# Performance work log

Hardware: AMD Instinct MI355X
Metric: run time of the kernel (lower is better)

Reference implementation:

```python
import jax, jax.numpy as jnp
import numpy as np

H = 1024  # hidden size

def lstm_cell(x, h, c, Wih, Whh, b):
    # torch gate order: i, f, g, o
    g = x @ Wih.T + h @ Whh.T + b
    i, f, gg, o = jnp.split(g, 4, axis=-1)
    c = jax.nn.sigmoid(f) * c + jax.nn.sigmoid(i) * jnp.tanh(gg)
    h = jax.nn.sigmoid(o) * jnp.tanh(c)
    return h, c

def lstm_layer(x, Wih, Whh, b):
    # x: [B, S, in] -> (y [B, S, H], h_last [B, H], c_last [B, H])
    B = x.shape[0]
    h0 = jnp.zeros((B, H), x.dtype)
    def step(carry, xt):
        h, c = carry
        h, c = lstm_cell(xt, h, c, Wih, Whh, b)
        return (h, c), h
    (h, c), ys = jax.lax.scan(step, (h0, h0), jnp.swapaxes(x, 0, 1))
    return jnp.swapaxes(ys, 0, 1), h, c

def setup_inputs() -> dict:
    key = jax.random.key(0)
    ks = iter(jax.random.split(key, 24))
    V, E, B, Ss, St = 32000, 512, 32, 64, 64
    s = 0.05
    d = {
        'source': jax.random.randint(next(ks), (B, Ss), 0, V),
        'prev_outputs': jax.random.randint(next(ks), (B, St), 0, V),
        'emb': jax.random.normal(next(ks), (V, E)) * s,
        'enc_Wih0': jax.random.normal(next(ks), (4*H, E)) * s,
        'enc_Whh0': jax.random.normal(next(ks), (4*H, H)) * s,
        'enc_b0': jax.random.normal(next(ks), (4*H,)) * s,
        'enc_Wih1': jax.random.normal(next(ks), (4*H, H)) * s,
        'enc_Whh1': jax.random.normal(next(ks), (4*H, H)) * s,
        'enc_b1': jax.random.normal(next(ks), (4*H,)) * s,
        'dec_Wih0': jax.random.normal(next(ks), (4*H, E + H)) * s,
        'dec_Whh0': jax.random.normal(next(ks), (4*H, H)) * s,
        'dec_b0': jax.random.normal(next(ks), (4*H,)) * s,
        'dec_Wih1': jax.random.normal(next(ks), (4*H, H)) * s,
        'dec_Whh1': jax.random.normal(next(ks), (4*H, H)) * s,
        'dec_b1': jax.random.normal(next(ks), (4*H,)) * s,
        'Wk': jax.random.normal(next(ks), (H, H)) * s,
        'bk': jax.random.normal(next(ks), (H,)) * s,
        'Wh': jax.random.normal(next(ks), (V, H)) * s,
        'bh': jax.random.normal(next(ks), (V,)) * s,
    }
    return d

def reference(source, prev_outputs, emb, enc_Wih0, enc_Whh0, enc_b0,
              enc_Wih1, enc_Whh1, enc_b1, dec_Wih0, dec_Whh0, dec_b0,
              dec_Wih1, dec_Whh1, dec_b1, Wk, bk, Wh, bh):
    src_e = emb[source]          # [B, Ss, E]
    tgt_e = emb[prev_outputs]    # [B, St, E]
    y0, h0e, c0e = lstm_layer(src_e, enc_Wih0, enc_Whh0, enc_b0)
    enc_out, h1e, c1e = lstm_layer(y0, enc_Wih1, enc_Whh1, enc_b1)
    h = jnp.stack([h0e, h1e])    # [L, B, H]
    c = jnp.stack([c0e, c1e])
    attn_key = enc_out @ Wk.T + bk  # constant across decoder steps

    def step(carry, xt):  # xt: [B, E]
        h, c = carry
        q = h[-1]                                        # [B, H]
        scores = jnp.einsum('bh,bsh->bs', q, attn_key)   # [B, Ss]
        probs = jax.nn.softmax(scores, axis=-1)
        ctx = jnp.einsum('bs,bsh->bh', probs, enc_out)   # [B, H]
        inp = jnp.concatenate([xt, ctx], axis=-1)        # [B, E+H]
        h0n, c0n = lstm_cell(inp, h[0], c[0], dec_Wih0, dec_Whh0, dec_b0)
        h1n, c1n = lstm_cell(h0n, h[1], c[1], dec_Wih1, dec_Whh1, dec_b1)
        logits_t = h1n @ Wh.T + bh                       # [B, V]
        return (jnp.stack([h0n, h1n]), jnp.stack([c0n, c1n])), logits_t

    _, logits = jax.lax.scan(step, (h, c), jnp.swapaxes(tgt_e, 0, 1))
    return jnp.swapaxes(logits, 0, 1)  # [B, St, V]
```

## Files before the change

### kernel.cpp

```cpp
#include <hip/hip_runtime.h>
#include <cmath>

typedef short bs8 __attribute__((ext_vector_type(8)));
typedef float f32x4 __attribute__((ext_vector_type(4)));
typedef __attribute__((address_space(3))) unsigned lds_uint;
typedef __attribute__((address_space(1))) const unsigned gbl_uint;

#define NV 32000
#define SLOTH (32 * 1024)

__device__ __forceinline__ float b2f(unsigned short u) {
  union { unsigned int i; float f; } v; v.i = ((unsigned int)u) << 16; return v.f;
}
__device__ __forceinline__ unsigned short f2b(float f) {
  unsigned int u = __float_as_uint(f);
  return (unsigned short)((u + 0x7FFFu + ((u >> 16) & 1u)) >> 16);
}
__device__ __forceinline__ f32x4 mfma16(bs8 a, bs8 b, f32x4 c) {
  return __builtin_amdgcn_mfma_f32_16x16x32_bf16(a, b, c, 0, 0, 0);
}

__device__ __forceinline__ void waitN(const unsigned* slots, int n, unsigned target) {
  if (threadIdx.x < 64) {
    for (;;) {
      unsigned mn = 0xffffffffu;
      for (int i = threadIdx.x; i < n; i += 64) {
        unsigned v = __hip_atomic_load(slots + (size_t)i * 4,
                                       __ATOMIC_RELAXED, __HIP_MEMORY_SCOPE_AGENT);
        mn = mn < v ? mn : v;
      }
#pragma unroll
      for (int off = 32; off; off >>= 1) {
        unsigned o = __shfl_xor(mn, off);
        mn = mn < o ? mn : o;
      }
      if (mn >= target) break;
      __builtin_amdgcn_s_sleep(2);
    }
  }
  __syncthreads();
}
__device__ __forceinline__ void signal_slot(unsigned* slot, unsigned val) {
  __syncthreads();
  if (threadIdx.x == 0)
    __hip_atomic_store(slot, val, __ATOMIC_RELAXED, __HIP_MEMORY_SCOPE_AGENT);
}

__device__ __forceinline__ void mfma_half8(
    const unsigned short* __restrict__ A, const unsigned short* __restrict__ W,
    int u0, f32x4& acc0, f32x4& acc1) {
  int tid = threadIdx.x;
  int w = tid >> 6, l = tid & 63;
  int col = l & 15;
  int kb = w * 128 + (l >> 4) * 8;
  size_t wrow = (size_t)(col >> 2) * 1024 + u0 + (col & 3);
  const unsigned short* ap = A + (size_t)col * 1024 + kb;
  const unsigned short* wp = W + wrow * 1024 + kb;
#pragma unroll
  for (int kk = 0; kk < 128; kk += 32) {
    bs8 b1 = *(const bs8*)(wp + kk);
    acc0 = mfma16(*(const bs8*)(ap + kk), b1, acc0);
    acc1 = mfma16(*(const bs8*)(ap + 16 * 1024 + kk), b1, acc1);
  }
}
__device__ __forceinline__ void red_write8(f32x4 acc0, f32x4 acc1, float (*red)[32][17]) {
  int tid = threadIdx.x;
  int w = tid >> 6, l = tid & 63, col = l & 15;
#pragma unroll
  for (int r = 0; r < 4; r++) {
    red[w][(l >> 4) * 4 + r][col] = acc0[r];
    red[w][16 + (l >> 4) * 4 + r][col] = acc1[r];
  }
  __syncthreads();
}
template <int NW, int AH>
__device__ __forceinline__ void cell_finish(
    int u0, float (*red)[32][17],
    const float* __restrict__ gxrow, const float* __restrict__ bias,
    const float* __restrict__ cprev,
    unsigned short* __restrict__ hout, float* __restrict__ cout) {
  int tid = threadIdx.x;
  if (tid < 128) {
    int b_ = tid >> 2, ul = tid & 3, u = u0 + ul;
    float s0 = 0.f, s1 = 0.f, s2 = 0.f, s3 = 0.f;
#pragma unroll
    for (int ww = 0; ww < NW; ww++) {
      s0 += red[ww][b_][ul];      s1 += red[ww][b_][4 + ul];
      s2 += red[ww][b_][8 + ul];  s3 += red[ww][b_][12 + ul];
    }
    if (gxrow) {
      const float* gp = gxrow + (size_t)b_ * 4096 + u;
      s0 += gp[0]; s1 += gp[1024]; s2 += gp[2048]; s3 += gp[3072];
    }
    if (bias) {
      s0 += bias[u]; s1 += bias[u + 1024]; s2 += bias[u + 2048]; s3 += bias[u + 3072];
    }
    float si = 1.f / (1.f + expf(-s0));
    float sf = 1.f / (1.f + expf(-s1));
    float tg = tanhf(s2);
    float so = 1.f / (1.f + expf(-s3));
    float cn = sf * cprev[b_ * 1024 + u] + si * tg;
    float hn = so * tanhf(cn);
    cout[b_ * 1024 + u] = cn;
    unsigned hv = (unsigned)f2b(hn);
    unsigned ho = __shfl_down(hv, 1);
    if (AH) {
      if (!(ul & 1)) {
        unsigned packed = hv | (ho << 16);
        __hip_atomic_store((unsigned*)hout + ((size_t)b_ * 512 + (u0 >> 1) + (ul >> 1)),
                           packed, __ATOMIC_RELAXED, __HIP_MEMORY_SCOPE_AGENT);
      }
    } else {
      hout[b_ * 1024 + u] = (unsigned short)hv;
    }
  }
}

__global__ __launch_bounds__(512) void enc_diag(
    int d,
    const unsigned short* __restrict__ wH0, const float* __restrict__ gx0,
    unsigned short* __restrict__ y0h, float* __restrict__ c0h,
    const unsigned short* __restrict__ wE1, const unsigned short* __restrict__ wH1,
    const float* __restrict__ eb1,
    unsigned short* __restrict__ y1h, float* __restrict__ c1h) {
  __shared__ float red[8][32][17];
  if (blockIdx.x < 256) {
    if (d >= 64) return;
    int u0 = blockIdx.x * 4;
    f32x4 a0 = {0.f, 0.f, 0.f, 0.f}, a1 = {0.f, 0.f, 0.f, 0.f};
    mfma_half8(y0h + (size_t)d * SLOTH, wH0, u0, a0, a1);
    red_write8(a0, a1, red);
    cell_finish<8, 0>(u0, red, gx0 + (size_t)d * 131072, nullptr,
                      c0h + (size_t)d * SLOTH,
                      y0h + (size_t)(d + 1) * SLOTH, c0h + (size_t)(d + 1) * SLOTH);
  } else {
    if (d < 1) return;
    int j = d - 1, u0 = (blockIdx.x - 256) * 4;
    f32x4 a0 = {0.f, 0.f, 0.f, 0.f}, a1 = {0.f, 0.f, 0.f, 0.f};
    mfma_half8(y0h + (size_t)(j + 1) * SLOTH, wE1, u0, a0, a1);
    mfma_half8(y1h + (size_t)j * SLOTH, wH1, u0, a0, a1);
    red_write8(a0, a1, red);
    cell_finish<8, 0>(u0, red, nullptr, eb1, c1h + (size_t)j * SLOTH,
                      y1h + (size_t)(j + 1) * SLOTH, c1h + (size_t)(j + 1) * SLOTH);
  }
}

__device__ __forceinline__ void mfma_half_lds(
    const unsigned short* __restrict__ A, const unsigned short* wl,
    f32x4& acc0, f32x4& acc1) {
  int tid = threadIdx.x;
  int w = tid >> 6, l = tid & 63;
  int col = l & 15;
  int kb = w * 256 + (l >> 4) * 8;
  const unsigned short* ap = A + (size_t)col * 1024 + kb;
  const unsigned short* wp = wl + col * 1032 + kb;
#pragma unroll
  for (int kk = 0; kk < 256; kk += 32) {
    bs8 b1 = *(const bs8*)(wp + kk);
    acc0 = mfma16(*(const bs8*)(ap + kk), b1, acc0);
    acc1 = mfma16(*(const bs8*)(ap + 16 * 1024 + kk), b1, acc1);
  }
}
__device__ __forceinline__ void red_write4(f32x4 acc0, f32x4 acc1, float (*red)[32][17]) {
  int tid = threadIdx.x;
  int w = tid >> 6, l = tid & 63, col = l & 15;
#pragma unroll
  for (int r = 0; r < 4; r++) {
    red[w][(l >> 4) * 4 + r][col] = acc0[r];
    red[w][16 + (l >> 4) * 4 + r][col] = acc1[r];
  }
  __syncthreads();
}

__global__ __launch_bounds__(256, 2) void dec_persist(
    const unsigned short* __restrict__ ak, const unsigned short* __restrict__ enc,
    const float* __restrict__ gxd,
    const unsigned short* __restrict__ wDh0, const unsigned short* __restrict__ wD0c,
    const unsigned short* __restrict__ wD1, const unsigned short* __restrict__ wDh1,
    const float* __restrict__ db1, unsigned short* __restrict__ ctxb,
    unsigned short* __restrict__ dh0, float* __restrict__ dc0,
    unsigned short* __restrict__ dh1, float* __restrict__ dc1,
    unsigned* __restrict__ flags) {
  __shared__ unsigned short wl[2][16 * 1032];
  __shared__ float red[4][32][17];
  __shared__ float qs[1024];
  __shared__ float sc[64];
  int bid = blockIdx.x, tid = threadIdx.x;
  int cell0 = (bid < 256);
  int u0 = (bid & 255) * 4;
  unsigned* fH0 = flags;
  unsigned* fH1 = flags + 1024;
  unsigned* fP  = flags + 2048;
  {
    const unsigned short* W0 = cell0 ? wDh0 : wD1;
    const unsigned short* W1 = cell0 ? wD0c : wDh1;
    for (int i = tid; i < 2048; i += 256) {
      int c = i >> 7, c8 = (i & 127) * 8;
      size_t grow = (size_t)(c >> 2) * 1024 + u0 + (c & 3);
      *(bs8*)&wl[0][c * 1032 + c8] = *(const bs8*)(W0 + grow * 1024 + c8);
      *(bs8*)&wl[1][c * 1032 + c8] = *(const bs8*)(W1 + grow * 1024 + c8);
    }
    __syncthreads();
  }
  if (cell0) {
    for (int t = 0; t < 64; t++) {
      if (t > 0) waitN(fH0, 256, (unsigned)t);
      f32x4 a0 = {0.f, 0.f, 0.f, 0.f}, a1 = {0.f, 0.f, 0.f, 0.f};
      mfma_half_lds(dh0 + (size_t)t * SLOTH, wl[0], a0, a1);
      waitN(fP, 32, (unsigned)(t + 1));
      mfma_half_lds(ctxb + (size_t)t * SLOTH, wl[1], a0, a1);
      red_write4(a0, a1, red);
      cell_finish<4, 1>(u0, red, gxd + (size_t)t * 131072, nullptr,
                        dc0 + (size_t)t * SLOTH,
                        dh0 + (size_t)(t + 1) * SLOTH, dc0 + (size_t)(t + 1) * SLOTH);
      signal_slot(fH0 + (size_t)bid * 4, (unsigned)(t + 1));
    }
  } else {
    int ab = bid - 256;
    for (int t = 0; t < 64; t++) {
      if (t > 0) waitN(fH1, 256, (unsigned)t);
      if (ab < 32) {
        {
          ushort4 u4 = *(const ushort4*)(dh1 + (size_t)t * SLOTH + (size_t)ab * 1024 + tid * 4);
          qs[tid * 4 + 0] = b2f(u4.x); qs[tid * 4 + 1] = b2f(u4.y);
          qs[tid * 4 + 2] = b2f(u4.z); qs[tid * 4 + 3] = b2f(u4.w);
        }
        __syncthreads();
        int w = tid >> 6, l = tid & 63;
        for (int ss = 0; ss < 16; ss++) {
          int s = w * 16 + ss;
          const unsigned short* kr = ak + (size_t)(s * 32 + ab) * 1024;
          float p = 0.f;
#pragma unroll
          for (int i = 0; i < 4; i++) {
            int e = (l + i * 64) * 4;
            ushort4 u4 = *(const ushort4*)&kr[e];
            p += qs[e] * b2f(u4.x) + qs[e + 1] * b2f(u4.y)
               + qs[e + 2] * b2f(u4.z) + qs[e + 3] * b2f(u4.w);
          }
          for (int off = 32; off; off >>= 1) p += __shfl_down(p, off);
          if (l == 0) sc[s] = p;
        }
        __syncthreads();
        if (tid < 64) {
          float v = sc[tid], m = v;
          for (int off = 32; off; off >>= 1) m = fmaxf(m, __shfl_xor(m, off));
          float e = expf(v - m), su = e;
          for (int off = 32; off; off >>= 1) su += __shfl_xor(su, off);
          sc[tid] = e / su;
        }
        __syncthreads();
        {
          int h4 = tid * 4;
          float a0 = 0.f, a1 = 0.f, a2 = 0.f, a3 = 0.f;
#pragma unroll 8
          for (int s = 0; s < 64; s++) {
            float p = sc[s];
            ushort4 u4 = *(const ushort4*)&enc[(size_t)(s * 32 + ab) * 1024 + h4];
            a0 += p * b2f(u4.x); a1 += p * b2f(u4.y);
            a2 += p * b2f(u4.z); a3 += p * b2f(u4.w);
          }
          unsigned* cp = (unsigned*)(ctxb + (size_t)t * SLOTH) + ab * 512 + tid * 2;
          __hip_atomic_store(cp, (unsigned)f2b(a0) | ((unsigned)f2b(a1) << 16),
                             __ATOMIC_RELAXED, __HIP_MEMORY_SCOPE_AGENT);
          __hip_atomic_store(cp + 1, (unsigned)f2b(a2) | ((unsigned)f2b(a3) << 16),
                             __ATOMIC_RELAXED, __HIP_MEMORY_SCOPE_AGENT);
        }
        signal_slot(fP + (size_t)ab * 4, (unsigned)(t + 1));
      }
      f32x4 a0 = {0.f, 0.f, 0.f, 0.f}, a1 = {0.f, 0.f, 0.f, 0.f};
      mfma_half_lds(dh1 + (size_t)t * SLOTH, wl[1], a0, a1);
      waitN(fH0, 256, (unsigned)(t + 1));
      mfma_half_lds(dh0 + (size_t)(t + 1) * SLOTH, wl[0], a0, a1);
      red_write4(a0, a1, red);
      cell_finish<4, 1>(u0, red, nullptr, db1, dc1 + (size_t)t * SLOTH,
                        dh1 + (size_t)(t + 1) * SLOTH, dc1 + (size_t)(t + 1) * SLOTH);
      signal_slot(fH1 + (size_t)(bid - 256) * 4, (unsigned)(t + 1));
    }
  }
}

struct CvtDesc { const float* src; unsigned short* dst; int total8, cols, ld, col0, blk0; };
struct CvtArgs { CvtDesc d[11]; };
__global__ __launch_bounds__(256) void cvt_all(CvtArgs a) {
  int blk = blockIdx.x, seg = 0;
#pragma unroll
  for (int i = 1; i < 11; i++) if (blk >= a.d[i].blk0) seg = i;
  CvtDesc d = a.d[seg];
  int idx = (blk - d.blk0) * 256 + threadIdx.x;
  if (idx >= d.total8) return;
  int cpr = d.cols >> 3;
  int r = idx / cpr, c8 = (idx - r * cpr) * 8;
  const float* s = d.src + (size_t)r * d.ld + d.col0 + c8;
  float4 x = *(const float4*)s, y = *(const float4*)(s + 4);
  unsigned short o[8] = {f2b(x.x), f2b(x.y), f2b(x.z), f2b(x.w),
                         f2b(y.x), f2b(y.y), f2b(y.z), f2b(y.w)};
  *(bs8*)(d.dst + (size_t)r * d.cols + c8) = *(bs8*)o;
}

__global__ __launch_bounds__(256) void embed_kernel(
    const int* __restrict__ src, const int* __restrict__ prev,
    const float* __restrict__ emb,
    unsigned short* __restrict__ se, unsigned short* __restrict__ te) {
  int idx = blockIdx.x * 256 + threadIdx.x;
  int half = idx >> 17;
  int r = (idx >> 6) & 2047, c8 = (idx & 63) * 8;
  int s = r >> 5, b = r & 31;
  const int* tok = half ? prev : src;
  unsigned short* dst = half ? te : se;
  int t = tok[b * 64 + s];
  const float* e = emb + (size_t)t * 512 + c8;
  float4 a = *(const float4*)e, bb = *(const float4*)(e + 4);
  unsigned short o[8] = {f2b(a.x), f2b(a.y), f2b(a.z), f2b(a.w),
                         f2b(bb.x), f2b(bb.y), f2b(bb.z), f2b(bb.w)};
  *(bs8*)(dst + (size_t)r * 512 + c8) = *(bs8*)o;
}

#define NFLAGS 4096
__global__ __launch_bounds__(256) void zero_init(
    unsigned short* y0h, unsigned short* y1h, float* c0h, float* c1h,
    unsigned* flags) {
  int i = blockIdx.x * 256 + threadIdx.x;
  y0h[i] = 0; y1h[i] = 0; c0h[i] = 0.f; c1h[i] = 0.f;
  if (i < NFLAGS) flags[i] = 0u;
}
__global__ __launch_bounds__(256) void init_dec(
    const unsigned short* __restrict__ y0f, const unsigned short* __restrict__ y1f,
    const float* __restrict__ c0f, const float* __restrict__ c1f,
    unsigned short* dh0, unsigned short* dh1, float* dc0, float* dc1) {
  int i = blockIdx.x * 256 + threadIdx.x;
  dh0[i] = y0f[i]; dh1[i] = y1f[i]; dc0[i] = c0f[i]; dc1[i] = c1f[i];
}

template <int OUTMODE>
__global__ __launch_bounds__(256) void gemm_bf16(
    const unsigned short* __restrict__ A, int lda,
    const unsigned short* __restrict__ B, int ldb,
    const float* __restrict__ bias, void* __restrict__ Cp, int ldc, int K) {
  __shared__ unsigned short As[128 * 64];
  __shared__ unsigned short Bs[128 * 64];
  int tid = threadIdx.x;
  int m0, n0;
  if (OUTMODE == 1) {
    int nwg = gridDim.x * gridDim.y;
    int orig = blockIdx.y * gridDim.x + blockIdx.x;
    int q = nwg >> 3;
    int wg = (orig & 7) * q + (orig >> 3);
    m0 = (wg % gridDim.x) * 128;
    n0 = (wg / gridDim.x) * 128;
  } else {
    m0 = blockIdx.x * 128; n0 = blockIdx.y * 128;
  }
  int w = tid >> 6, l = tid & 63;
  int wr = w >> 1, wc = w & 1;
  int swz = ((l & 7) * 8) ^ ((l >> 3) * 8);
  f32x4 acc[4][4];
#pragma unroll
  for (int i = 0; i < 4; i++)
#pragma unroll
    for (int j = 0; j < 4; j++)
#pragma unroll
      for (int r = 0; r < 4; r++) acc[i][j][r] = 0.f;

  for (int k0 = 0; k0 < K; k0 += 64) {
    __syncthreads();
#pragma unroll
    for (int i = 0; i < 4; i++) {
      int rb = w * 8 + i * 32;
      const unsigned short* ga = A + (size_t)(m0 + rb + (l >> 3)) * lda + k0 + swz;
      __builtin_amdgcn_global_load_lds((gbl_uint*)ga, (lds_uint*)&As[rb * 64], 16, 0, 0);
      const unsigned short* gb = B + (size_t)(n0 + rb + (l >> 3)) * ldb + k0 + swz;
      __builtin_amdgcn_global_load_lds((gbl_uint*)gb, (lds_uint*)&Bs[rb * 64], 16, 0, 0);
    }
    __syncthreads();
#pragma unroll
    for (int kk = 0; kk < 2; kk++) {
      bs8 af[4], bfr[4];
#pragma unroll
      for (int i = 0; i < 4; i++) {
        int R = wr * 64 + i * 16 + (l & 15);
        af[i] = *(const bs8*)&As[R * 64 + ((kk * 32 + (l >> 4) * 8) ^ ((R & 7) * 8))];
      }
#pragma unroll
      for (int j = 0; j < 4; j++) {
        int R = wc * 64 + j * 16 + (l & 15);
        bfr[j] = *(const bs8*)&Bs[R * 64 + ((kk * 32 + (l >> 4) * 8) ^ ((R & 7) * 8))];
      }
#pragma unroll
      for (int i = 0; i < 4; i++)
#pragma unroll
        for (int j = 0; j < 4; j++)
          acc[i][j] = mfma16(af[i], bfr[j], acc[i][j]);
    }
  }
#pragma unroll
  for (int i = 0; i < 4; i++) {
    int mrow = m0 + wr * 64 + i * 16 + (l >> 4) * 4;
#pragma unroll
    for (int j = 0; j < 4; j++) {
      int n = n0 + wc * 64 + j * 16 + (l & 15);
      float bb = bias ? bias[n] : 0.f;
#pragma unroll
      for (int r = 0; r < 4; r++) {
        int m = mrow + r;
        float v = acc[i][j][r] + bb;
        if (OUTMODE == 1)
          ((float*)Cp)[(size_t)(m & 31) * (64ull * NV) + (size_t)(m >> 5) * NV + n] = v;
        else if (OUTMODE == 2)
          ((unsigned short*)Cp)[(size_t)m * ldc + n] = f2b(v);
        else
          ((float*)Cp)[(size_t)m * ldc + n] = v;
      }
    }
  }
}

extern "C" void kernel_launch(void* const* d_in, const int* in_sizes, int n_in,
                              void* d_out, int out_size, void* d_ws, size_t ws_size,
                              hipStream_t stream) {
  (void)in_sizes; (void)n_in; (void)out_size; (void)ws_size;
  const int*   src   = (const int*)d_in[0];
  const int*   prev  = (const int*)d_in[1];
  const float* emb   = (const float*)d_in[2];
  const float* eWih0 = (const float*)d_in[3];
  const float* eWhh0 = (const float*)d_in[4];
  const float* eb0   = (const float*)d_in[5];
  const float* eWih1 = (const float*)d_in[6];
  const float* eWhh1 = (const float*)d_in[7];
  const float* eb1   = (const float*)d_in[8];
  const float* dWih0 = (const float*)d_in[9];
  const float* dWhh0 = (const float*)d_in[10];
  const float* db0   = (const float*)d_in[11];
  const float* dWih1 = (const float*)d_in[12];
  const float* dWhh1 = (const float*)d_in[13];
  const float* db1   = (const float*)d_in[14];
  const float* Wk    = (const float*)d_in[15];
  const float* bk    = (const float*)d_in[16];
  const float* Wh    = (const float*)d_in[17];
  const float* bh    = (const float*)d_in[18];
  float* out = (float*)d_out;

  char* p = (char*)d_ws;
  auto alloc = [&](size_t bytes) {
    char* r = p; p += (bytes + 255) & ~(size_t)255; return r;
  };
  float* gx0 = (float*)alloc(2048ull * 4096 * 4);
  float* gxd = (float*)alloc(2048ull * 4096 * 4);
  float* c0h = (float*)alloc(65ull * SLOTH * 4);
  float* c1h = (float*)alloc(65ull * SLOTH * 4);
  float* dc0 = (float*)alloc(65ull * SLOTH * 4);
  float* dc1 = (float*)alloc(65ull * SLOTH * 4);
  unsigned short* y0h  = (unsigned short*)alloc(65ull * SLOTH * 2);
  unsigned short* y1h  = (unsigned short*)alloc(65ull * SLOTH * 2);
  unsigned short* dh0  = (unsigned short*)alloc(65ull * SLOTH * 2);
  unsigned short* dh1  = (unsigned short*)alloc(65ull * SLOTH * 2);
  unsigned short* ctxb = (unsigned short*)alloc(64ull * SLOTH * 2);
  unsigned short* se   = (unsigned short*)alloc(2048ull * 512 * 2);
  unsigned short* te   = (unsigned short*)alloc(2048ull * 512 * 2);
  unsigned short* ak   = (unsigned short*)alloc(2048ull * 1024 * 2);
  unsigned short* wE0  = (unsigned short*)alloc(4096ull * 512 * 2);
  unsigned short* wH0  = (unsigned short*)alloc(4096ull * 1024 * 2);
  unsigned short* wE1  = (unsigned short*)alloc(4096ull * 1024 * 2);
  unsigned short* wH1  = (unsigned short*)alloc(4096ull * 1024 * 2);
  unsigned short* wD0x = (unsigned short*)alloc(4096ull * 512 * 2);
  unsigned short* wD0c = (unsigned short*)alloc(4096ull * 1024 * 2);
  unsigned short* wDh0 = (unsigned short*)alloc(4096ull * 1024 * 2);
  unsigned short* wD1  = (unsigned short*)alloc(4096ull * 1024 * 2);
  unsigned short* wDh1 = (unsigned short*)alloc(4096ull * 1024 * 2);
  unsigned short* wK   = (unsigned short*)alloc(1024ull * 1024 * 2);
  unsigned short* wV   = (unsigned short*)alloc((size_t)NV * 1024 * 2);
  unsigned* flags = (unsigned*)alloc((size_t)NFLAGS * 4);

  CvtArgs ca; int nb = 0, ci = 0;
  auto addcvt = [&](const float* s, unsigned short* d, int rows, int cols, int ld, int c0) {
    int t8 = rows * cols / 8;
    ca.d[ci++] = CvtDesc{s, d, t8, cols, ld, c0, nb};
    nb += (t8 + 255) / 256;
  };
  addcvt(eWih0, wE0, 4096, 512, 512, 0);
  addcvt(eWhh0, wH0, 4096, 1024, 1024, 0);
  addcvt(eWih1, wE1, 4096, 1024, 1024, 0);
  addcvt(eWhh1, wH1, 4096, 1024, 1024, 0);
  addcvt(dWih0, wD0x, 4096, 512, 1536, 0);
  addcvt(dWih0, wD0c, 4096, 1024, 1536, 512);
  addcvt(dWhh0, wDh0, 4096, 1024, 1024, 0);
  addcvt(dWih1, wD1, 4096, 1024, 1024, 0);
  addcvt(dWhh1, wDh1, 4096, 1024, 1024, 0);
  addcvt(Wk, wK, 1024, 1024, 1024, 0);
  addcvt(Wh, wV, NV, 1024, 1024, 0);
  cvt_all<<<nb, 256, 0, stream>>>(ca);

  zero_init<<<128, 256, 0, stream>>>(y0h, y1h, c0h, c1h, flags);
  embed_kernel<<<1024, 256, 0, stream>>>(src, prev, emb, se, te);

  gemm_bf16<0><<<dim3(16, 32), 256, 0, stream>>>(se, 512, wE0, 512, eb0, gx0, 4096, 512);
  gemm_bf16<0><<<dim3(16, 32), 256, 0, stream>>>(te, 512, wD0x, 512, db0, gxd, 4096, 512);

  for (int d = 0; d <= 64; d++)
    enc_diag<<<512, 512, 0, stream>>>(d, wH0, gx0, y0h, c0h, wE1, wH1, eb1, y1h, c1h);

  gemm_bf16<2><<<dim3(16, 8), 256, 0, stream>>>(y1h + SLOTH, 1024, wK, 1024, bk, ak, 1024, 1024);
  init_dec<<<128, 256, 0, stream>>>(y0h + 64 * SLOTH, y1h + 64 * SLOTH,
                                    c0h + 64 * SLOTH, c1h + 64 * SLOTH,
                                    dh0, dh1, dc0, dc1);
  dec_persist<<<512, 256, 0, stream>>>(ak, y1h + SLOTH, gxd, wDh0, wD0c, wD1, wDh1,
                                       db1, ctxb, dh0, dc0, dh1, dc1, flags);
  gemm_bf16<1><<<dim3(16, 250), 256, 0, stream>>>(dh1 + SLOTH, 1024, wV, 1024, bh, out, NV, 1024);
}
```

Before: 2.800 ms.

## Split decoder batch into two 16-row cohorts with separate flags to pipeline steps

The persistent decoder kernel now processes the 32-row batch as two independent cohorts of 16 rows. Each cohort has its own ready flags for layer-0 hidden, layer-1 hidden and the attention context. Each cohort's matmul, gate activation and signal can proceed as soon as its own inputs are ready, so the attention and the next layer can start on cohort A while cohort B is still in flight. The cost is twice as many flag waits and signals, plus block barriers per step, and each MFMA pass reuses the loaded weights across fewer rows.

```diff
diff --git a/kernel.cpp b/kernel.cpp
--- a/kernel.cpp
+++ b/kernel.cpp
@@ -145,31 +145,63 @@
   }
 }
 
-__device__ __forceinline__ void mfma_half_lds(
+__device__ __forceinline__ void mfma_cohort(
     const unsigned short* __restrict__ A, const unsigned short* wl,
-    f32x4& acc0, f32x4& acc1) {
+    int X, f32x4& acc) {
   int tid = threadIdx.x;
   int w = tid >> 6, l = tid & 63;
   int col = l & 15;
   int kb = w * 256 + (l >> 4) * 8;
-  const unsigned short* ap = A + (size_t)col * 1024 + kb;
+  const unsigned short* ap = A + (size_t)(X * 16 + col) * 1024 + kb;
   const unsigned short* wp = wl + col * 1032 + kb;
 #pragma unroll
-  for (int kk = 0; kk < 256; kk += 32) {
-    bs8 b1 = *(const bs8*)(wp + kk);
-    acc0 = mfma16(*(const bs8*)(ap + kk), b1, acc0);
-    acc1 = mfma16(*(const bs8*)(ap + 16 * 1024 + kk), b1, acc1);
-  }
-}
-__device__ __forceinline__ void red_write4(f32x4 acc0, f32x4 acc1, float (*red)[32][17]) {
+  for (int kk = 0; kk < 256; kk += 32)
+    acc = mfma16(*(const bs8*)(ap + kk), *(const bs8*)(wp + kk), acc);
+}
+__device__ __forceinline__ void red_write1(f32x4 acc, float (*red)[16][17]) {
   int tid = threadIdx.x;
   int w = tid >> 6, l = tid & 63, col = l & 15;
 #pragma unroll
-  for (int r = 0; r < 4; r++) {
-    red[w][(l >> 4) * 4 + r][col] = acc0[r];
-    red[w][16 + (l >> 4) * 4 + r][col] = acc1[r];
-  }
+  for (int r = 0; r < 4; r++) red[w][(l >> 4) * 4 + r][col] = acc[r];
   __syncthreads();
+}
+__device__ __forceinline__ void finish16(
+    int u0, int X, float (*red)[16][17],
+    const float* __restrict__ gxrow, const float* __restrict__ bias,
+    const float* __restrict__ cprev,
+    unsigned short* __restrict__ hout, float* __restrict__ cout) {
+  int tid = threadIdx.x;
+  if (tid < 64) {
+    int b_ = tid >> 2, ul = tid & 3, u = u0 + ul;
+    int bm = X * 16 + b_;
+    float s0 = 0.f, s1 = 0.f, s2 = 0.f, s3 = 0.f;
+#pragma unroll
+    for (int ww = 0; ww < 4; ww++) {
+      s0 += red[ww][b_][ul];      s1 += red[ww][b_][4 + ul];
+      s2 += red[ww][b_][8 + ul];  s3 += red[ww][b_][12 + ul];
+    }
+    if (gxrow) {
+      const float* gp = gxrow + (size_t)bm * 4096 + u;
+      s0 += gp[0]; s1 += gp[1024]; s2 += gp[2048]; s3 += gp[3072];
+    }
+    if (bias) {
+      s0 += bias[u]; s1 += bias[u + 1024]; s2 += bias[u + 2048]; s3 += bias[u + 3072];
+    }
+    float si = 1.f / (1.f + expf(-s0));
+    float sf = 1.f / (1.f + expf(-s1));
+    float tg = tanhf(s2);
+    float so = 1.f / (1.f + expf(-s3));
+    float cn = sf * cprev[bm * 1024 + u] + si * tg;
+    float hn = so * tanhf(cn);
+    cout[bm * 1024 + u] = cn;
+    unsigned hv = (unsigned)f2b(hn);
+    unsigned ho = __shfl_down(hv, 1);
+    if (!(ul & 1)) {
+      unsigned packed = hv | (ho << 16);
+      __hip_atomic_store((unsigned*)hout + ((size_t)bm * 512 + (u0 >> 1) + (ul >> 1)),
+                         packed, __ATOMIC_RELAXED, __HIP_MEMORY_SCOPE_AGENT);
+    }
+  }
 }
 
 __global__ __launch_bounds__(256, 2) void dec_persist(
@@ -182,15 +214,18 @@
     unsigned short* __restrict__ dh1, float* __restrict__ dc1,
     unsigned* __restrict__ flags) {
   __shared__ unsigned short wl[2][16 * 1032];
-  __shared__ float red[4][32][17];
+  __shared__ float red[4][16][17];
   __shared__ float qs[1024];
   __shared__ float sc[64];
   int bid = blockIdx.x, tid = threadIdx.x;
   int cell0 = (bid < 256);
   int u0 = (bid & 255) * 4;
-  unsigned* fH0 = flags;
-  unsigned* fH1 = flags + 1024;
-  unsigned* fP  = flags + 2048;
+  unsigned* fH0A = flags;
+  unsigned* fH0B = flags + 1024;
+  unsigned* fH1A = flags + 2048;
+  unsigned* fH1B = flags + 3072;
+  unsigned* fPA  = flags + 4096;
+  unsigned* fPB  = flags + 4160;
   {
     const unsigned short* W0 = cell0 ? wDh0 : wD1;
     const unsigned short* W1 = cell0 ? wD0c : wDh1;
@@ -204,22 +239,32 @@
   }
   if (cell0) {
     for (int t = 0; t < 64; t++) {
-      if (t > 0) waitN(fH0, 256, (unsigned)t);
-      f32x4 a0 = {0.f, 0.f, 0.f, 0.f}, a1 = {0.f, 0.f, 0.f, 0.f};
-      mfma_half_lds(dh0 + (size_t)t * SLOTH, wl[0], a0, a1);
-      waitN(fP, 32, (unsigned)(t + 1));
-      mfma_half_lds(ctxb + (size_t)t * SLOTH, wl[1], a0, a1);
-      red_write4(a0, a1, red);
-      cell_finish<4, 1>(u0, red, gxd + (size_t)t * 131072, nullptr,
-                        dc0 + (size_t)t * SLOTH,
-                        dh0 + (size_t)(t + 1) * SLOTH, dc0 + (size_t)(t + 1) * SLOTH);
-      signal_slot(fH0 + (size_t)bid * 4, (unsigned)(t + 1));
+      f32x4 accA = {0.f, 0.f, 0.f, 0.f}, accB = {0.f, 0.f, 0.f, 0.f};
+      if (t > 0) waitN(fH0A, 256, (unsigned)t);
+      mfma_cohort(dh0 + (size_t)t * SLOTH, wl[0], 0, accA);
+      if (t > 0) waitN(fH0B, 256, (unsigned)t);
+      mfma_cohort(dh0 + (size_t)t * SLOTH, wl[0], 1, accB);
+      waitN(fPA, 16, (unsigned)(t + 1));
+      mfma_cohort(ctxb + (size_t)t * SLOTH, wl[1], 0, accA);
+      red_write1(accA, red);
+      finish16(u0, 0, red, gxd + (size_t)t * 131072, nullptr,
+               dc0 + (size_t)t * SLOTH,
+               dh0 + (size_t)(t + 1) * SLOTH, dc0 + (size_t)(t + 1) * SLOTH);
+      signal_slot(fH0A + (size_t)bid * 4, (unsigned)(t + 1));
+      waitN(fPB, 16, (unsigned)(t + 1));
+      mfma_cohort(ctxb + (size_t)t * SLOTH, wl[1], 1, accB);
+      red_write1(accB, red);
+      finish16(u0, 1, red, gxd + (size_t)t * 131072, nullptr,
+               dc0 + (size_t)t * SLOTH,
+               dh0 + (size_t)(t + 1) * SLOTH, dc0 + (size_t)(t + 1) * SLOTH);
+      signal_slot(fH0B + (size_t)bid * 4, (unsigned)(t + 1));
     }
   } else {
     int ab = bid - 256;
     for (int t = 0; t < 64; t++) {
-      if (t > 0) waitN(fH1, 256, (unsigned)t);
       if (ab < 32) {
+        unsigned* fH1X = (ab < 16) ? fH1A : fH1B;
+        waitN(fH1X, 256, (unsigned)t);
         {
           ushort4 u4 = *(const ushort4*)(dh1 + (size_t)t * SLOTH + (size_t)ab * 1024 + tid * 4);
           qs[tid * 4 + 0] = b2f(u4.x); qs[tid * 4 + 1] = b2f(u4.y);
@@ -266,16 +311,26 @@
           __hip_atomic_store(cp + 1, (unsigned)f2b(a2) | ((unsigned)f2b(a3) << 16),
                              __ATOMIC_RELAXED, __HIP_MEMORY_SCOPE_AGENT);
         }
-        signal_slot(fP + (size_t)ab * 4, (unsigned)(t + 1));
-      }
-      f32x4 a0 = {0.f, 0.f, 0.f, 0.f}, a1 = {0.f, 0.f, 0.f, 0.f};
-      mfma_half_lds(dh1 + (size_t)t * SLOTH, wl[1], a0, a1);
-      waitN(fH0, 256, (unsigned)(t + 1));
-      mfma_half_lds(dh0 + (size_t)(t + 1) * SLOTH, wl[0], a0, a1);
-      red_write4(a0, a1, red);
-      cell_finish<4, 1>(u0, red, nullptr, db1, dc1 + (size_t)t * SLOTH,
-                        dh1 + (size_t)(t + 1) * SLOTH, dc1 + (size_t)(t + 1) * SLOTH);
-      signal_slot(fH1 + (size_t)(bid - 256) * 4, (unsigned)(t + 1));
+        unsigned* fPX = (ab < 16) ? fPA : fPB;
+        signal_slot(fPX + (size_t)(ab & 15) * 4, (unsigned)(t + 1));
+      }
+      f32x4 accA = {0.f, 0.f, 0.f, 0.f}, accB = {0.f, 0.f, 0.f, 0.f};
+      if (t > 0) waitN(fH1A, 256, (unsigned)t);
+      mfma_cohort(dh1 + (size_t)t * SLOTH, wl[1], 0, accA);
+      if (t > 0) waitN(fH1B, 256, (unsigned)t);
+      mfma_cohort(dh1 + (size_t)t * SLOTH, wl[1], 1, accB);
+      waitN(fH0A, 256, (unsigned)(t + 1));
+      mfma_cohort(dh0 + (size_t)(t + 1) * SLOTH, wl[0], 0, accA);
+      red_write1(accA, red);
+      finish16(u0, 0, red, nullptr, db1, dc1 + (size_t)t * SLOTH,
+               dh1 + (size_t)(t + 1) * SLOTH, dc1 + (size_t)(t + 1) * SLOTH);
+      signal_slot(fH1A + (size_t)(bid - 256) * 4, (unsigned)(t + 1));
+      waitN(fH0B, 256, (unsigned)(t + 1));
+      mfma_cohort(dh0 + (size_t)(t + 1) * SLOTH, wl[0], 1, accB);
+      red_write1(accB, red);
+      finish16(u0, 1, red, nullptr, db1, dc1 + (size_t)t * SLOTH,
+               dh1 + (size_t)(t + 1) * SLOTH, dc1 + (size_t)(t + 1) * SLOTH);
+      signal_slot(fH1B + (size_t)(bid - 256) * 4, (unsigned)(t + 1));
     }
   }
 }
@@ -316,7 +371,7 @@
   *(bs8*)(dst + (size_t)r * 512 + c8) = *(bs8*)o;
 }
 
-#define NFLAGS 4096
+#define NFLAGS 4224
 __global__ __launch_bounds__(256) void zero_init(
     unsigned short* y0h, unsigned short* y1h, float* c0h, float* c1h,
     unsigned* flags) {
```

After: 2.838 ms. Within noise of the previous version (+1.4%).

## Replace per-step encoder kernel launches with a persistent flag-synchronized kernel

Applied to the files above, without the earlier changes.

The encoder wavefront, which used 65 separate kernel launches each holding a diagonal step, becomes one persistent kernel. Each block caches its slice of the recurrent weights in LDS once and then synchronizes step-to-step through global flag counters, using the same scheme the decoder already uses. This removes launch overhead and the per-step weight reloads from global memory. In exchange it relies on all 512 blocks being co-resident (two per CU) and adds spin-wait polling, which risks deadlock if occupancy falls short.

```diff
diff --git a/kernel.cpp b/kernel.cpp
--- a/kernel.cpp
+++ b/kernel.cpp
@@ -46,24 +46,23 @@
     __hip_atomic_store(slot, val, __ATOMIC_RELAXED, __HIP_MEMORY_SCOPE_AGENT);
 }
 
-__device__ __forceinline__ void mfma_half8(
-    const unsigned short* __restrict__ A, const unsigned short* __restrict__ W,
-    int u0, f32x4& acc0, f32x4& acc1) {
+__device__ __forceinline__ void mfma_half_lds(
+    const unsigned short* __restrict__ A, const unsigned short* wl,
+    f32x4& acc0, f32x4& acc1) {
   int tid = threadIdx.x;
   int w = tid >> 6, l = tid & 63;
   int col = l & 15;
-  int kb = w * 128 + (l >> 4) * 8;
-  size_t wrow = (size_t)(col >> 2) * 1024 + u0 + (col & 3);
+  int kb = w * 256 + (l >> 4) * 8;
   const unsigned short* ap = A + (size_t)col * 1024 + kb;
-  const unsigned short* wp = W + wrow * 1024 + kb;
-#pragma unroll
-  for (int kk = 0; kk < 128; kk += 32) {
+  const unsigned short* wp = wl + col * 1032 + kb;
+#pragma unroll
+  for (int kk = 0; kk < 256; kk += 32) {
     bs8 b1 = *(const bs8*)(wp + kk);
     acc0 = mfma16(*(const bs8*)(ap + kk), b1, acc0);
     acc1 = mfma16(*(const bs8*)(ap + 16 * 1024 + kk), b1, acc1);
   }
 }
-__device__ __forceinline__ void red_write8(f32x4 acc0, f32x4 acc1, float (*red)[32][17]) {
+__device__ __forceinline__ void red_write4(f32x4 acc0, f32x4 acc1, float (*red)[32][17]) {
   int tid = threadIdx.x;
   int w = tid >> 6, l = tid & 63, col = l & 15;
 #pragma unroll
@@ -73,8 +72,7 @@
   }
   __syncthreads();
 }
-template <int NW, int AH>
-__device__ __forceinline__ void cell_finish(
+__device__ __forceinline__ void cell_finish4(
     int u0, float (*red)[32][17],
     const float* __restrict__ gxrow, const float* __restrict__ bias,
     const float* __restrict__ cprev,
@@ -84,7 +82,7 @@
     int b_ = tid >> 2, ul = tid & 3, u = u0 + ul;
     float s0 = 0.f, s1 = 0.f, s2 = 0.f, s3 = 0.f;
 #pragma unroll
-    for (int ww = 0; ww < NW; ww++) {
+    for (int ww = 0; ww < 4; ww++) {
       s0 += red[ww][b_][ul];      s1 += red[ww][b_][4 + ul];
       s2 += red[ww][b_][8 + ul];  s3 += red[ww][b_][12 + ul];
     }
@@ -104,72 +102,61 @@
     cout[b_ * 1024 + u] = cn;
     unsigned hv = (unsigned)f2b(hn);
     unsigned ho = __shfl_down(hv, 1);
-    if (AH) {
-      if (!(ul & 1)) {
-        unsigned packed = hv | (ho << 16);
-        __hip_atomic_store((unsigned*)hout + ((size_t)b_ * 512 + (u0 >> 1) + (ul >> 1)),
-                           packed, __ATOMIC_RELAXED, __HIP_MEMORY_SCOPE_AGENT);
-      }
-    } else {
-      hout[b_ * 1024 + u] = (unsigned short)hv;
-    }
-  }
-}
-
-__global__ __launch_bounds__(512) void enc_diag(
-    int d,
+    if (!(ul & 1)) {
+      unsigned packed = hv | (ho << 16);
+      __hip_atomic_store((unsigned*)hout + ((size_t)b_ * 512 + (u0 >> 1) + (ul >> 1)),
+                         packed, __ATOMIC_RELAXED, __HIP_MEMORY_SCOPE_AGENT);
+    }
+  }
+}
+
+__global__ __launch_bounds__(256, 2) void enc_persist(
     const unsigned short* __restrict__ wH0, const float* __restrict__ gx0,
     unsigned short* __restrict__ y0h, float* __restrict__ c0h,
     const unsigned short* __restrict__ wE1, const unsigned short* __restrict__ wH1,
     const float* __restrict__ eb1,
-    unsigned short* __restrict__ y1h, float* __restrict__ c1h) {
-  __shared__ float red[8][32][17];
-  if (blockIdx.x < 256) {
-    if (d >= 64) return;
-    int u0 = blockIdx.x * 4;
-    f32x4 a0 = {0.f, 0.f, 0.f, 0.f}, a1 = {0.f, 0.f, 0.f, 0.f};
-    mfma_half8(y0h + (size_t)d * SLOTH, wH0, u0, a0, a1);
-    red_write8(a0, a1, red);
-    cell_finish<8, 0>(u0, red, gx0 + (size_t)d * 131072, nullptr,
-                      c0h + (size_t)d * SLOTH,
-                      y0h + (size_t)(d + 1) * SLOTH, c0h + (size_t)(d + 1) * SLOTH);
+    unsigned short* __restrict__ y1h, float* __restrict__ c1h,
+    unsigned* __restrict__ fE, unsigned* __restrict__ fF) {
+  __shared__ unsigned short wl[2][16 * 1032];
+  __shared__ float red[4][32][17];
+  int bid = blockIdx.x, tid = threadIdx.x;
+  int lay0 = (bid < 256);
+  int u0 = (bid & 255) * 4;
+  {
+    const unsigned short* W0 = lay0 ? wH0 : wE1;
+    const unsigned short* W1 = lay0 ? wH0 : wH1;
+    for (int i = tid; i < 2048; i += 256) {
+      int c = i >> 7, c8 = (i & 127) * 8;
+      size_t grow = (size_t)(c >> 2) * 1024 + u0 + (c & 3);
+      *(bs8*)&wl[0][c * 1032 + c8] = *(const bs8*)(W0 + grow * 1024 + c8);
+      *(bs8*)&wl[1][c * 1032 + c8] = *(const bs8*)(W1 + grow * 1024 + c8);
+    }
+    __syncthreads();
+  }
+  if (lay0) {
+    for (int d = 0; d < 64; d++) {
+      if (d > 0) waitN(fE, 256, (unsigned)d);
+      f32x4 a0 = {0.f, 0.f, 0.f, 0.f}, a1 = {0.f, 0.f, 0.f, 0.f};
+      mfma_half_lds(y0h + (size_t)d * SLOTH, wl[0], a0, a1);
+      red_write4(a0, a1, red);
+      cell_finish4(u0, red, gx0 + (size_t)d * 131072, nullptr,
+                   c0h + (size_t)d * SLOTH,
+                   y0h + (size_t)(d + 1) * SLOTH, c0h + (size_t)(d + 1) * SLOTH);
+      signal_slot(fE + (size_t)bid * 4, (unsigned)(d + 1));
+    }
   } else {
-    if (d < 1) return;
-    int j = d - 1, u0 = (blockIdx.x - 256) * 4;
-    f32x4 a0 = {0.f, 0.f, 0.f, 0.f}, a1 = {0.f, 0.f, 0.f, 0.f};
-    mfma_half8(y0h + (size_t)(j + 1) * SLOTH, wE1, u0, a0, a1);
-    mfma_half8(y1h + (size_t)j * SLOTH, wH1, u0, a0, a1);
-    red_write8(a0, a1, red);
-    cell_finish<8, 0>(u0, red, nullptr, eb1, c1h + (size_t)j * SLOTH,
-                      y1h + (size_t)(j + 1) * SLOTH, c1h + (size_t)(j + 1) * SLOTH);
-  }
-}
-
-__device__ __forceinline__ void mfma_half_lds(
-    const unsigned short* __restrict__ A, const unsigned short* wl,
-    f32x4& acc0, f32x4& acc1) {
-  int tid = threadIdx.x;
-  int w = tid >> 6, l = tid & 63;
-  int col = l & 15;
-  int kb = w * 256 + (l >> 4) * 8;
-  const unsigned short* ap = A + (size_t)col * 1024 + kb;
-  const unsigned short* wp = wl + col * 1032 + kb;
-#pragma unroll
-  for (int kk = 0; kk < 256; kk += 32) {
-    bs8 b1 = *(const bs8*)(wp + kk);
-    acc0 = mfma16(*(const bs8*)(ap + kk), b1, acc0);
-    acc1 = mfma16(*(const bs8*)(ap + 16 * 1024 + kk), b1, acc1);
-  }
-}
-__device__ __forceinline__ void red_write4(f32x4 acc0, f32x4 acc1, float (*red)[32][17]) {
-  int tid = threadIdx.x;
-  int w = tid >> 6, l = tid & 63, col = l & 15;
-#pragma unroll
-  for (int r = 0; r < 4; r++) {
-    red[w][(l >> 4) * 4 + r][col] = acc0[r];
-    red[w][16 + (l >> 4) * 4 + r][col] = acc1[r];
-  }
-  __syncthreads();
+    for (int j = 0; j < 64; j++) {
+      waitN(fE, 256, (unsigned)(j + 1));
+      if (j > 0) waitN(fF, 256, (unsigned)j);
+      f32x4 a0 = {0.f, 0.f, 0.f, 0.f}, a1 = {0.f, 0.f, 0.f, 0.f};
+      mfma_half_lds(y0h + (size_t)(j + 1) * SLOTH, wl[0], a0, a1);
+      mfma_half_lds(y1h + (size_t)j * SLOTH, wl[1], a0, a1);
+      red_write4(a0, a1, red);
+      cell_finish4(u0, red, nullptr, eb1, c1h + (size_t)j * SLOTH,
+                   y1h + (size_t)(j + 1) * SLOTH, c1h + (size_t)(j + 1) * SLOTH);
+      signal_slot(fF + (size_t)(bid - 256) * 4, (unsigned)(j + 1));
+    }
+  }
 }
 
 __global__ __launch_bounds__(256, 2) void dec_persist(
@@ -210,9 +197,9 @@
       waitN(fP, 32, (unsigned)(t + 1));
       mfma_half_lds(ctxb + (size_t)t * SLOTH, wl[1], a0, a1);
       red_write4(a0, a1, red);
-      cell_finish<4, 1>(u0, red, gxd + (size_t)t * 131072, nullptr,
-                        dc0 + (size_t)t * SLOTH,
-                        dh0 + (size_t)(t + 1) * SLOTH, dc0 + (size_t)(t + 1) * SLOTH);
+      cell_finish4(u0, red, gxd + (size_t)t * 131072, nullptr,
+                   dc0 + (size_t)t * SLOTH,
+                   dh0 + (size_t)(t + 1) * SLOTH, dc0 + (size_t)(t + 1) * SLOTH);
       signal_slot(fH0 + (size_t)bid * 4, (unsigned)(t + 1));
     }
   } else {
@@ -273,8 +260,8 @@
       waitN(fH0, 256, (unsigned)(t + 1));
       mfma_half_lds(dh0 + (size_t)(t + 1) * SLOTH, wl[0], a0, a1);
       red_write4(a0, a1, red);
-      cell_finish<4, 1>(u0, red, nullptr, db1, dc1 + (size_t)t * SLOTH,
-                        dh1 + (size_t)(t + 1) * SLOTH, dc1 + (size_t)(t + 1) * SLOTH);
+      cell_finish4(u0, red, nullptr, db1, dc1 + (size_t)t * SLOTH,
+                   dh1 + (size_t)(t + 1) * SLOTH, dc1 + (size_t)(t + 1) * SLOTH);
       signal_slot(fH1 + (size_t)(bid - 256) * 4, (unsigned)(t + 1));
     }
   }
@@ -316,7 +303,7 @@
   *(bs8*)(dst + (size_t)r * 512 + c8) = *(bs8*)o;
 }
 
-#define NFLAGS 4096
+#define NFLAGS 6272
 __global__ __launch_bounds__(256) void zero_init(
     unsigned short* y0h, unsigned short* y1h, float* c0h, float* c1h,
     unsigned* flags) {
@@ -470,6 +457,8 @@
   unsigned short* wK   = (unsigned short*)alloc(1024ull * 1024 * 2);
   unsigned short* wV   = (unsigned short*)alloc((size_t)NV * 1024 * 2);
   unsigned* flags = (unsigned*)alloc((size_t)NFLAGS * 4);
+  unsigned* fE = flags + 4224;
+  unsigned* fF = flags + 5248;
 
   CvtArgs ca; int nb = 0, ci = 0;
   auto addcvt = [&](const float* s, unsigned short* d, int rows, int cols, int ld, int c0) {
@@ -496,8 +485,8 @@
   gemm_bf16<0><<<dim3(16, 32), 256, 0, stream>>>(se, 512, wE0, 512, eb0, gx0, 4096, 512);
   gemm_bf16<0><<<dim3(16, 32), 256, 0, stream>>>(te, 512, wD0x, 512, db0, gxd, 4096, 512);
 
-  for (int d = 0; d <= 64; d++)
-    enc_diag<<<512, 512, 0, stream>>>(d, wH0, gx0, y0h, c0h, wE1, wH1, eb1, y1h, c1h);
+  enc_persist<<<512, 256, 0, stream>>>(wH0, gx0, y0h, c0h, wE1, wH1, eb1,
+                                       y1h, c1h, fE, fF);
 
   gemm_bf16<2><<<dim3(16, 8), 256, 0, stream>>>(y1h + SLOTH, 1024, wK, 1024, bk, ak, 1024, 1024);
   init_dec<<<128, 256, 0, stream>>>(y0h + 64 * SLOTH, y1h + 64 * SLOTH,
```

New measurement: 2.644 ms. 1.06x faster.
